# Performance work log

Measured on AMD Instinct MI355X. Metric: run time of the kernel, lower is better.

Reference implementation:

```python
import jax, jax.numpy as jnp
import numpy as np

# (multiplicity, 2l+1) for irreps 128x0e + 64x1e + 32x2e
MUL = [(128, 1), (64, 3), (32, 5)]
N_SPECIES = 89
N_NODES = 100000


def setup_inputs() -> dict:
    key = jax.random.key(0)
    k = jax.random.split(key, 5)
    dim_x = sum(m * d for m, d in MUL)  # 480
    x = jax.random.normal(k[0], (N_NODES, dim_x), jnp.float32)
    z = jax.random.normal(k[1], (N_NODES, N_SPECIES), jnp.float32)
    # FullyConnectedTensorProduct path weights: one [mul_x, mul_z, mul_out] block per l
    w0 = jax.random.normal(k[2], (128, N_SPECIES, 128), jnp.float32)
    w1 = jax.random.normal(k[3], (64, N_SPECIES, 64), jnp.float32)
    w2 = jax.random.normal(k[4], (32, N_SPECIES, 32), jnp.float32)
    return {"x": x, "z": z, "w0": w0, "w1": w1, "w2": w2}


def _fctp(x, z, weights):
    # FullyConnectedTensorProduct with an all-scalar (0e) operand:
    # single matching-l path; CG reduces to identity over m and the e3nn
    # path normalization is alpha = 1/sqrt(fan_in) = 1/sqrt(mul_x * mul_z).
    outs = []
    off = 0
    n_z = z.shape[1]
    for (mul, d), w in zip(MUL, weights):
        xs = x[:, off:off + mul * d].reshape(-1, mul, d)  # [n, u, m]
        alpha = np.float32(1.0 / np.sqrt(mul * n_z))
        o = jnp.einsum('num,nv,uvw->nwm', xs, z, w) * alpha
        outs.append(o.reshape(-1, w.shape[2] * d))
        off += mul * d
    return jnp.concatenate(outs, axis=1)


def reference(x, z, w0, w1, w2):
    return _fctp(x, z, (w0, w1, w2))
```

## Files before the change

kernel.cpp:

```cpp
#include <hip/hip_runtime.h>
#include <hip/hip_bf16.h>
#include <math.h>


typedef __attribute__((ext_vector_type(8))) short short8;
typedef __attribute__((ext_vector_type(4))) float float4v;

static constexpr int N_FEAT = 480;

__device__ __forceinline__ unsigned short f2bf(float v) {
    __hip_bfloat16 h = __float2bfloat16(v);
    return __builtin_bit_cast(unsigned short, h);
}

template<int U>
__global__ void pack_w_kernel(const float* __restrict__ w, unsigned short* __restrict__ wb) {
    const int total = U * U * 96;
    int i = blockIdx.x * 256 + threadIdx.x;
    if (i >= total) return;
    int v = i % 96;
    int uw = i / 96;
    int wcol = uw % U;
    int u = uw / U;
    float val = (v < 89) ? w[(u * 89 + v) * U + wcol] : 0.0f;
    wb[i] = f2bf(val);
}

template<int U, int D, int WSUB, int OFF>
__global__ __launch_bounds__(256, 2)
void fctp_kernel(const float* __restrict__ x, const float* __restrict__ z,
                 const unsigned short* __restrict__ wb, float* __restrict__ out,
                 int nN, float alpha) {
    constexpr int C = U * D;
    __shared__ unsigned short xlds[C][132];

    const int tid  = threadIdx.x;
    const int lane = tid & 63;
    const int wave = tid >> 6;
    const int q    = lane >> 4;
    const int c    = lane & 15;
    const int wn   = wave >> 1;
    const int ww   = wave & 1;

    const int nbase = blockIdx.x * 128;
    const int wbase = blockIdx.y * (2 * WSUB * 16) + ww * (WSUB * 16);
    const int nwave = nbase + wn * 64;

    for (int e = tid; e < 128 * C; e += 256) {
        int nl = e / C;
        int cc = e - nl * C;
        int ng = nbase + nl;
        float v = (ng < nN) ? x[ng * N_FEAT + OFF + cc] : 0.0f;
        xlds[cc][nl] = f2bf(v);
    }

    short8 afrag[4][3];
#pragma unroll
    for (int nt = 0; nt < 4; ++nt) {
        int ng = nwave + nt * 16 + c;
        if (ng >= nN) ng = nN - 1;
        const float* zrow = z + ng * 89;
#pragma unroll
        for (int kk = 0; kk < 3; ++kk) {
            short8 f;
#pragma unroll
            for (int j = 0; j < 8; ++j) {
                int v = kk * 32 + q * 8 + j;
                float val = (v < 89) ? zrow[v] : 0.0f;
                f[j] = (short)f2bf(val);
            }
            afrag[nt][kk] = f;
        }
    }
    __syncthreads();

    float4v oacc[4][WSUB][D];
#pragma unroll
    for (int nt = 0; nt < 4; ++nt)
#pragma unroll
        for (int wt = 0; wt < WSUB; ++wt)
#pragma unroll
            for (int m = 0; m < D; ++m)
                oacc[nt][wt][m] = float4v{0.f, 0.f, 0.f, 0.f};

    const unsigned short* wptr[WSUB];
#pragma unroll
    for (int wt = 0; wt < WSUB; ++wt)
        wptr[wt] = wb + (wbase + wt * 16 + c) * 96 + q * 8;

    short8 bfr[2][WSUB][3];
#pragma unroll
    for (int wt = 0; wt < WSUB; ++wt)
#pragma unroll
        for (int kk = 0; kk < 3; ++kk)
            bfr[0][wt][kk] = *reinterpret_cast<const short8*>(wptr[wt] + kk * 32);

#pragma unroll 2
    for (int u = 0; u < U; ++u) {
        const int cur = u & 1, nxt = cur ^ 1;
        const int un = (u + 1 < U) ? (u + 1) : u;
#pragma unroll
        for (int wt = 0; wt < WSUB; ++wt)
#pragma unroll
            for (int kk = 0; kk < 3; ++kk)
                bfr[nxt][wt][kk] = *reinterpret_cast<const short8*>(wptr[wt] + un * (U * 96) + kk * 32);

        float4v t[4][WSUB];
#pragma unroll
        for (int nt = 0; nt < 4; ++nt)
#pragma unroll
            for (int wt = 0; wt < WSUB; ++wt) {
                float4v acc = {0.f, 0.f, 0.f, 0.f};
                acc = __builtin_amdgcn_mfma_f32_16x16x32_bf16(afrag[nt][0], bfr[cur][wt][0], acc, 0, 0, 0);
                acc = __builtin_amdgcn_mfma_f32_16x16x32_bf16(afrag[nt][1], bfr[cur][wt][1], acc, 0, 0, 0);
                acc = __builtin_amdgcn_mfma_f32_16x16x32_bf16(afrag[nt][2], bfr[cur][wt][2], acc, 0, 0, 0);
                t[nt][wt] = acc;
            }

#pragma unroll
        for (int nt = 0; nt < 4; ++nt) {
#pragma unroll
            for (int m = 0; m < D; ++m) {
                const unsigned short* p = &xlds[u * D + m][wn * 64 + nt * 16 + q * 4];
                uint2 xv = *reinterpret_cast<const uint2*>(p);
                float xf[4];
                xf[0] = __uint_as_float(xv.x << 16);
                xf[1] = __uint_as_float(xv.x & 0xffff0000u);
                xf[2] = __uint_as_float(xv.y << 16);
                xf[3] = __uint_as_float(xv.y & 0xffff0000u);
#pragma unroll
                for (int wt = 0; wt < WSUB; ++wt)
#pragma unroll
                    for (int r = 0; r < 4; ++r)
                        oacc[nt][wt][m][r] += t[nt][wt][r] * xf[r];
            }
        }
    }

#pragma unroll
    for (int nt = 0; nt < 4; ++nt)
#pragma unroll
        for (int wt = 0; wt < WSUB; ++wt) {
            const int wg = wbase + wt * 16 + c;
#pragma unroll
            for (int r = 0; r < 4; ++r) {
                const int ng = nwave + nt * 16 + q * 4 + r;
                if (ng < nN) {
#pragma unroll
                    for (int m = 0; m < D; ++m)
                        out[ng * N_FEAT + OFF + wg * D + m] = alpha * oacc[nt][wt][m][r];
                }
            }
        }
}

extern "C" void kernel_launch(void* const* d_in, const int* in_sizes, int n_in,
                              void* d_out, int out_size, void* d_ws, size_t ws_size,
                              hipStream_t stream) {
    const float* x  = (const float*)d_in[0];
    const float* z  = (const float*)d_in[1];
    const float* w0 = (const float*)d_in[2];
    const float* w1 = (const float*)d_in[3];
    const float* w2 = (const float*)d_in[4];
    float* out = (float*)d_out;
    const int N = in_sizes[0] / N_FEAT;

    unsigned short* wb0 = (unsigned short*)d_ws;
    unsigned short* wb1 = wb0 + 128 * 128 * 96;
    unsigned short* wb2 = wb1 + 64 * 64 * 96;

    pack_w_kernel<128><<<(128 * 128 * 96 + 255) / 256, 256, 0, stream>>>(w0, wb0);
    pack_w_kernel<64><<<(64 * 64 * 96 + 255) / 256, 256, 0, stream>>>(w1, wb1);
    pack_w_kernel<32><<<(32 * 32 * 96 + 255) / 256, 256, 0, stream>>>(w2, wb2);

    const int nblocks = (N + 127) / 128;
    const float a0 = 1.0f / sqrtf(128.0f * 89.0f);
    const float a1 = 1.0f / sqrtf(64.0f * 89.0f);
    const float a2 = 1.0f / sqrtf(32.0f * 89.0f);

    fctp_kernel<128, 1, 2, 0><<<dim3(nblocks, 2), 256, 0, stream>>>(x, z, wb0, out, N, a0);
    fctp_kernel<64, 3, 1, 128><<<dim3(nblocks, 2), 256, 0, stream>>>(x, z, wb1, out, N, a1);
    fctp_kernel<32, 5, 1, 320><<<dim3(nblocks, 1), 256, 0, stream>>>(x, z, wb2, out, N, a2);
}
```

Baseline: 1.049 ms.

## Transpose MFMA operands, keep x in fp32 LDS rows, retile blocks per node

Swaps the MFMA operand order so each lane holds one node and four consecutive output columns, which allows vectorized float4 stores to output rows. The x slice is staged in LDS as fp32 using float4 global loads instead of a bf16 transposed layout, which removes the bf16 rounding of x. Blocks now cover 64 nodes and all output columns, with per-irrep NT/WT tiling, and the launch bound is raised to 3 blocks per CU. This trades larger LDS per node and more blocks for coalesced loads and stores and better occupancy.

```diff
diff --git a/kernel.cpp b/kernel.cpp
--- a/kernel.cpp
+++ b/kernel.cpp
@@ -26,38 +26,42 @@
     wb[i] = f2bf(val);
 }
 
-template<int U, int D, int WSUB, int OFF>
-__global__ __launch_bounds__(256, 2)
+template<int U, int D, int NT, int WT, int OFF>
+__global__ __launch_bounds__(256, 3)
 void fctp_kernel(const float* __restrict__ x, const float* __restrict__ z,
                  const unsigned short* __restrict__ wb, float* __restrict__ out,
                  int nN, float alpha) {
-    constexpr int C = U * D;
-    __shared__ unsigned short xlds[C][132];
+    constexpr int C  = U * D;
+    constexpr int SP = C + 4;
+    constexpr int GN = 64 / (NT * 16);
+    __shared__ float xlds[64 * SP];
 
     const int tid  = threadIdx.x;
     const int lane = tid & 63;
     const int wave = tid >> 6;
     const int q    = lane >> 4;
     const int c    = lane & 15;
-    const int wn   = wave >> 1;
-    const int ww   = wave & 1;
+    const int wn   = wave % GN;
+    const int ww   = wave / GN;
+    const int nbase = blockIdx.x * 64;
 
-    const int nbase = blockIdx.x * 128;
-    const int wbase = blockIdx.y * (2 * WSUB * 16) + ww * (WSUB * 16);
-    const int nwave = nbase + wn * 64;
-
-    for (int e = tid; e < 128 * C; e += 256) {
-        int nl = e / C;
-        int cc = e - nl * C;
+    constexpr int CQ = C / 4;
+#pragma unroll
+    for (int it = 0; it < C / 16; ++it) {
+        int e  = it * 256 + tid;
+        int nl = e / CQ;
+        int cq = e - nl * CQ;
         int ng = nbase + nl;
-        float v = (ng < nN) ? x[ng * N_FEAT + OFF + cc] : 0.0f;
-        xlds[cc][nl] = f2bf(v);
+        float4v v = {0.f, 0.f, 0.f, 0.f};
+        if (ng < nN)
+            v = *reinterpret_cast<const float4v*>(x + ng * N_FEAT + OFF + cq * 4);
+        *reinterpret_cast<float4v*>(&xlds[nl * SP + cq * 4]) = v;
     }
 
-    short8 afrag[4][3];
+    short8 zfr[NT][3];
 #pragma unroll
-    for (int nt = 0; nt < 4; ++nt) {
-        int ng = nwave + nt * 16 + c;
+    for (int nt = 0; nt < NT; ++nt) {
+        int ng = nbase + wn * (NT * 16) + nt * 16 + c;
         if (ng >= nN) ng = nN - 1;
         const float* zrow = z + ng * 89;
 #pragma unroll
@@ -69,28 +73,28 @@
                 float val = (v < 89) ? zrow[v] : 0.0f;
                 f[j] = (short)f2bf(val);
             }
-            afrag[nt][kk] = f;
+            zfr[nt][kk] = f;
         }
     }
     __syncthreads();
 
-    float4v oacc[4][WSUB][D];
+    float4v oacc[NT][WT][D];
 #pragma unroll
-    for (int nt = 0; nt < 4; ++nt)
+    for (int nt = 0; nt < NT; ++nt)
 #pragma unroll
-        for (int wt = 0; wt < WSUB; ++wt)
+        for (int wt = 0; wt < WT; ++wt)
 #pragma unroll
             for (int m = 0; m < D; ++m)
                 oacc[nt][wt][m] = float4v{0.f, 0.f, 0.f, 0.f};
 
-    const unsigned short* wptr[WSUB];
+    const unsigned short* wptr[WT];
 #pragma unroll
-    for (int wt = 0; wt < WSUB; ++wt)
-        wptr[wt] = wb + (wbase + wt * 16 + c) * 96 + q * 8;
+    for (int wt = 0; wt < WT; ++wt)
+        wptr[wt] = wb + (ww * (WT * 16) + wt * 16 + c) * 96 + q * 8;
 
-    short8 bfr[2][WSUB][3];
+    short8 bfr[2][WT][3];
 #pragma unroll
-    for (int wt = 0; wt < WSUB; ++wt)
+    for (int wt = 0; wt < WT; ++wt)
 #pragma unroll
         for (int kk = 0; kk < 3; ++kk)
             bfr[0][wt][kk] = *reinterpret_cast<const short8*>(wptr[wt] + kk * 32);
@@ -100,58 +104,54 @@
         const int cur = u & 1, nxt = cur ^ 1;
         const int un = (u + 1 < U) ? (u + 1) : u;
 #pragma unroll
-        for (int wt = 0; wt < WSUB; ++wt)
+        for (int wt = 0; wt < WT; ++wt)
 #pragma unroll
             for (int kk = 0; kk < 3; ++kk)
                 bfr[nxt][wt][kk] = *reinterpret_cast<const short8*>(wptr[wt] + un * (U * 96) + kk * 32);
 
-        float4v t[4][WSUB];
+        float xv[NT][D];
 #pragma unroll
-        for (int nt = 0; nt < 4; ++nt)
+        for (int nt = 0; nt < NT; ++nt)
 #pragma unroll
-            for (int wt = 0; wt < WSUB; ++wt) {
-                float4v acc = {0.f, 0.f, 0.f, 0.f};
-                acc = __builtin_amdgcn_mfma_f32_16x16x32_bf16(afrag[nt][0], bfr[cur][wt][0], acc, 0, 0, 0);
-                acc = __builtin_amdgcn_mfma_f32_16x16x32_bf16(afrag[nt][1], bfr[cur][wt][1], acc, 0, 0, 0);
-                acc = __builtin_amdgcn_mfma_f32_16x16x32_bf16(afrag[nt][2], bfr[cur][wt][2], acc, 0, 0, 0);
-                t[nt][wt] = acc;
-            }
+            for (int m = 0; m < D; ++m)
+                xv[nt][m] = xlds[(wn * (NT * 16) + nt * 16 + c) * SP + u * D + m];
 
 #pragma unroll
-        for (int nt = 0; nt < 4; ++nt) {
+        for (int nt = 0; nt < NT; ++nt)
 #pragma unroll
-            for (int m = 0; m < D; ++m) {
-                const unsigned short* p = &xlds[u * D + m][wn * 64 + nt * 16 + q * 4];
-                uint2 xv = *reinterpret_cast<const uint2*>(p);
-                float xf[4];
-                xf[0] = __uint_as_float(xv.x << 16);
-                xf[1] = __uint_as_float(xv.x & 0xffff0000u);
-                xf[2] = __uint_as_float(xv.y << 16);
-                xf[3] = __uint_as_float(xv.y & 0xffff0000u);
+            for (int wt = 0; wt < WT; ++wt) {
+                float4v acc = {0.f, 0.f, 0.f, 0.f};
+                acc = __builtin_amdgcn_mfma_f32_16x16x32_bf16(bfr[cur][wt][0], zfr[nt][0], acc, 0, 0, 0);
+                acc = __builtin_amdgcn_mfma_f32_16x16x32_bf16(bfr[cur][wt][1], zfr[nt][1], acc, 0, 0, 0);
+                acc = __builtin_amdgcn_mfma_f32_16x16x32_bf16(bfr[cur][wt][2], zfr[nt][2], acc, 0, 0, 0);
 #pragma unroll
-                for (int wt = 0; wt < WSUB; ++wt)
+                for (int m = 0; m < D; ++m)
 #pragma unroll
                     for (int r = 0; r < 4; ++r)
-                        oacc[nt][wt][m][r] += t[nt][wt][r] * xf[r];
+                        oacc[nt][wt][m][r] += acc[r] * xv[nt][m];
             }
-        }
     }
 
 #pragma unroll
-    for (int nt = 0; nt < 4; ++nt)
+    for (int nt = 0; nt < NT; ++nt) {
+        const int node = nbase + wn * (NT * 16) + nt * 16 + c;
+        if (node >= nN) continue;
 #pragma unroll
-        for (int wt = 0; wt < WSUB; ++wt) {
-            const int wg = wbase + wt * 16 + c;
+        for (int wt = 0; wt < WT; ++wt) {
+            const int w0 = ww * (WT * 16) + wt * 16 + q * 4;
+            float vals[4 * D];
 #pragma unroll
-            for (int r = 0; r < 4; ++r) {
-                const int ng = nwave + nt * 16 + q * 4 + r;
-                if (ng < nN) {
+            for (int r = 0; r < 4; ++r)
 #pragma unroll
-                    for (int m = 0; m < D; ++m)
-                        out[ng * N_FEAT + OFF + wg * D + m] = alpha * oacc[nt][wt][m][r];
-                }
-            }
+                for (int m = 0; m < D; ++m)
+                    vals[r * D + m] = alpha * oacc[nt][wt][m][r];
+            float* o = out + node * N_FEAT + OFF + w0 * D;
+#pragma unroll
+            for (int j = 0; j < D; ++j)
+                *reinterpret_cast<float4v*>(o + j * 4) =
+                    float4v{vals[j * 4 + 0], vals[j * 4 + 1], vals[j * 4 + 2], vals[j * 4 + 3]};
         }
+    }
 }
 
 extern "C" void kernel_launch(void* const* d_in, const int* in_sizes, int n_in,
@@ -173,12 +173,12 @@
     pack_w_kernel<64><<<(64 * 64 * 96 + 255) / 256, 256, 0, stream>>>(w1, wb1);
     pack_w_kernel<32><<<(32 * 32 * 96 + 255) / 256, 256, 0, stream>>>(w2, wb2);
 
-    const int nblocks = (N + 127) / 128;
+    const int nblocks = (N + 63) / 64;
     const float a0 = 1.0f / sqrtf(128.0f * 89.0f);
     const float a1 = 1.0f / sqrtf(64.0f * 89.0f);
     const float a2 = 1.0f / sqrtf(32.0f * 89.0f);
 
-    fctp_kernel<128, 1, 2, 0><<<dim3(nblocks, 2), 256, 0, stream>>>(x, z, wb0, out, N, a0);
-    fctp_kernel<64, 3, 1, 128><<<dim3(nblocks, 2), 256, 0, stream>>>(x, z, wb1, out, N, a1);
-    fctp_kernel<32, 5, 1, 320><<<dim3(nblocks, 1), 256, 0, stream>>>(x, z, wb2, out, N, a2);
+    fctp_kernel<128, 1, 4, 2, 0><<<nblocks, 256, 0, stream>>>(x, z, wb0, out, N, a0);
+    fctp_kernel<64, 3, 2, 2, 128><<<nblocks, 256, 0, stream>>>(x, z, wb1, out, N, a1);
+    fctp_kernel<32, 5, 1, 2, 320><<<nblocks, 256, 0, stream>>>(x, z, wb2, out, N, a2);
 }
```

Result: faster. 947.3 us (-9.7%).
